# Performance work log

Hardware: AMD Instinct MI355X
Metric: run time of the kernel (lower is better)

Reference implementation:

```python
import jax, jax.numpy as jnp
import numpy as np

EPS = 1e-08


def _glorot(key, shape):
    fan_in, fan_out = shape[0], shape[1]
    lim = jnp.sqrt(6.0 / (fan_in + fan_out)).astype(jnp.float32)
    return jax.random.uniform(key, shape, jnp.float32, -lim, lim)


def setup_inputs() -> dict:
    key = jax.random.key(0)
    ks = jax.random.split(key, 12)
    n_nodes, n_edges, nf, hid = 50000, 1600000, 64, 64
    x = jax.random.normal(ks[0], (n_nodes, 3), jnp.float32)
    hh = jax.random.normal(ks[1], (n_nodes, nf), jnp.float32)
    src_idx = jax.random.randint(ks[2], (n_edges,), 0, n_nodes)
    dst_idx = jax.random.randint(ks[3], (n_edges,), 0, n_nodes)
    in_edge = 2 * nf + 1  # radial (1) + src hh + dst hh
    params = {
        "W1": _glorot(ks[4], (in_edge, hid)), "b1": jnp.zeros((hid,), jnp.float32),
        "W2": _glorot(ks[5], (hid, hid)),     "b2": jnp.zeros((hid,), jnp.float32),
        "W3": _glorot(ks[6], (hid, hid)),     "b3": jnp.zeros((hid,), jnp.float32),
        # final coord layer: xavier_uniform with gain 0.001, no bias
        "W4": _glorot(ks[7], (hid, 1)) * 0.001,
    }
    return {"x": x, "hh": hh, "src_idx": src_idx, "dst_idx": dst_idx, **params}


def reference(x, hh, src_idx, dst_idx, W1, b1, W2, b2, W3, b3, W4):
    # gather per-edge endpoint data
    xs, xd = x[src_idx], x[dst_idx]              # [E,3]
    coord_diff = xs - xd                         # [E,3]
    radial = jnp.sum(coord_diff * coord_diff, axis=1, keepdims=True)  # [E,1]

    # edge MLP: Linear -> SiLU -> Linear -> SiLU
    ef = jnp.concatenate([radial, hh[src_idx], hh[dst_idx]], axis=1)  # [E, 2*nf+1]
    ef = jax.nn.silu(ef @ W1 + b1)
    edge_feature = jax.nn.silu(ef @ W2 + b2)     # [E, hid]

    # normalize coord_diff by detached distance (normalize=True)
    norm = jax.lax.stop_gradient(jnp.sqrt(radial)) + EPS
    coord_diff = coord_diff / norm

    # coord MLP: Linear -> SiLU -> Linear(hid,1,no bias) -> Tanh (tanh=True)
    scale = jnp.tanh(jax.nn.silu(edge_feature @ W3 + b3) @ W4)  # [E,1]
    trans = coord_diff * scale                   # [E,3]
    return radial, trans, edge_feature
```

## Files before the change

kernel.cpp:

```cpp
#include <hip/hip_runtime.h>
#include <math.h>

typedef _Float16 f16x8 __attribute__((ext_vector_type(8)));
typedef __fp16   pk16x2 __attribute__((ext_vector_type(2)));
typedef float    f32x16 __attribute__((ext_vector_type(16)));
typedef float    f32x4  __attribute__((ext_vector_type(4)));
typedef unsigned int u32x4 __attribute__((ext_vector_type(4)));

__device__ __forceinline__ float silu_f(float v) {
  return v * __builtin_amdgcn_rcpf(1.0f + __expf(-v));
}
__device__ __forceinline__ float tanh_fast(float x) {
  return 1.0f - 2.0f * __builtin_amdgcn_rcpf(__expf(2.0f * x) + 1.0f);
}

__device__ __forceinline__ unsigned pkrtz(float a, float b) {
  pk16x2 h = __builtin_amdgcn_cvt_pkrtz(a, b);
  return __builtin_bit_cast(unsigned, h);
}
__device__ __forceinline__ void plswap(unsigned &a, unsigned &b) {
  asm volatile("v_permlane32_swap_b32 %0, %1" : "+v"(a), "+v"(b));
}
__device__ __forceinline__ f16x8 frag4(unsigned r0, unsigned r1, unsigned r2, unsigned r3) {
  u32x4 u = {r0, r1, r2, r3};
  return __builtin_bit_cast(f16x8, u);
}
__device__ __forceinline__ f32x16 zero16() {
  f32x16 z;
  #pragma unroll
  for (int i = 0; i < 16; ++i) z[i] = 0.0f;
  return z;
}

#define NFRAG 38

__global__ __launch_bounds__(512, 8) void egnn_edge_kernel(
    const float* __restrict__ x,
    const float* __restrict__ hh,
    const int* __restrict__ src_idx,
    const int* __restrict__ dst_idx,
    const float* __restrict__ W1, const float* __restrict__ b1,
    const float* __restrict__ W2, const float* __restrict__ b2,
    const float* __restrict__ W3, const float* __restrict__ b3,
    const float* __restrict__ W4,
    float* __restrict__ out_radial,
    float* __restrict__ out_trans,
    float* __restrict__ out_ef,
    int n_edges)
{
    __shared__ __align__(16) unsigned short sA[NFRAG * 512];
    __shared__ float sW4f[64];

    const int tid = threadIdx.x;

    for (int idx = tid; idx < NFRAG * 64; idx += 512) {
        const int f = idx >> 6, l = idx & 63;
        const int fhi = l >> 5, row = l & 31;
        int layer, m, t;
        if (f < 18)      { layer = 1; m = f / 9;        t = f % 9; }
        else if (f < 28) { layer = 2; m = (f - 18) / 5; t = (f - 18) % 5; }
        else             { layer = 3; m = (f - 28) / 5; t = (f - 28) % 5; }
        const int row_out = m * 32 + row;
        #pragma unroll
        for (int j = 0; j < 8; ++j) {
            const int kf = t * 16 + fhi * 8 + j;
            float v = 0.0f;
            if (layer == 1) {
                if (kf < 128)       v = W1[(1 + kf) * 64 + row_out];
                else if (kf == 128) v = W1[row_out];
                else if (kf == 136) v = b1[row_out];
            } else {
                const float* W = (layer == 2) ? W2 : W3;
                const float* b = (layer == 2) ? b2 : b3;
                if (kf < 64)       v = W[kf * 64 + row_out];
                else if (kf == 64) v = b[row_out];
            }
            sA[f * 512 + l * 8 + j] = __builtin_bit_cast(unsigned short, (_Float16)v);
        }
    }
    for (int i = tid; i < 64; i += 512) {
        const int fhi = i >> 5, k = i & 31;
        const int m = k >> 4, r = k & 15;
        sW4f[i] = W4[m * 32 + (r & 3) + 8 * (r >> 2) + 4 * fhi];
    }
    __syncthreads();

    const int lane = tid & 63;
    const int c  = lane & 31;
    const int hi = lane >> 5;
    const int wave = tid >> 6;
    const unsigned short* myA = sA + lane * 8;

    const long ngrp = ((long)n_edges + 31) >> 5;
    const long wid  = (long)blockIdx.x * 8 + wave;
    const long wtot = (long)gridDim.x * 8;

    for (long g = wid; g < ngrp; g += wtot) {
        const long eidx = g * 32 + c;
        const long e = (eidx < n_edges) ? eidx : (long)n_edges - 1;
        const bool valid = (eidx < n_edges);
        const int s = src_idx[e];
        const int d = dst_idx[e];

        const float dx0 = x[3*s+0] - x[3*d+0];
        const float dx1 = x[3*s+1] - x[3*d+1];
        const float dx2 = x[3*s+2] - x[3*d+2];
        const float radial = dx0*dx0 + dx1*dx1 + dx2*dx2;

        const float4* hsp = reinterpret_cast<const float4*>(hh + (long)s * 64 + hi * 8);
        const float4* hdp = reinterpret_cast<const float4*>(hh + (long)d * 64 + hi * 8);
        unsigned B1[9][4];
        #pragma unroll
        for (int t = 0; t < 4; ++t) {
            float4 a = hsp[4*t], b = hsp[4*t + 1];
            B1[t][0] = pkrtz(a.x, a.y); B1[t][1] = pkrtz(a.z, a.w);
            B1[t][2] = pkrtz(b.x, b.y); B1[t][3] = pkrtz(b.z, b.w);
            float4 p = hdp[4*t], q = hdp[4*t + 1];
            B1[4+t][0] = pkrtz(p.x, p.y); B1[4+t][1] = pkrtz(p.z, p.w);
            B1[4+t][2] = pkrtz(q.x, q.y); B1[4+t][3] = pkrtz(q.z, q.w);
        }
        B1[8][0] = hi ? 0x00003C00u : pkrtz(radial, 0.0f);
        B1[8][1] = 0u; B1[8][2] = 0u; B1[8][3] = 0u;

        f32x16 acc0 = zero16(), acc1 = zero16();
        #pragma unroll
        for (int t = 0; t < 9; ++t) {
            f16x8 bt = frag4(B1[t][0], B1[t][1], B1[t][2], B1[t][3]);
            acc0 = __builtin_amdgcn_mfma_f32_32x32x16_f16(
                *(const f16x8*)(myA + (t)     * 512), bt, acc0, 0, 0, 0);
            acc1 = __builtin_amdgcn_mfma_f32_32x32x16_f16(
                *(const f16x8*)(myA + (9 + t) * 512), bt, acc1, 0, 0, 0);
        }
        f32x16 s0, s1;
        #pragma unroll
        for (int r = 0; r < 16; ++r) { s0[r] = silu_f(acc0[r]); s1[r] = silu_f(acc1[r]); }

        unsigned B2[4][4];
        #pragma unroll
        for (int tt = 0; tt < 2; ++tt) {
            unsigned L0 = pkrtz(s0[8*tt+0], s0[8*tt+1]), L1 = pkrtz(s0[8*tt+2], s0[8*tt+3]);
            unsigned H0 = pkrtz(s0[8*tt+4], s0[8*tt+5]), H1 = pkrtz(s0[8*tt+6], s0[8*tt+7]);
            plswap(L0, H0); plswap(L1, H1);
            B2[tt][0] = L0; B2[tt][1] = L1; B2[tt][2] = H0; B2[tt][3] = H1;
            unsigned M0 = pkrtz(s1[8*tt+0], s1[8*tt+1]), M1 = pkrtz(s1[8*tt+2], s1[8*tt+3]);
            unsigned N0 = pkrtz(s1[8*tt+4], s1[8*tt+5]), N1 = pkrtz(s1[8*tt+6], s1[8*tt+7]);
            plswap(M0, N0); plswap(M1, N1);
            B2[2+tt][0] = M0; B2[2+tt][1] = M1; B2[2+tt][2] = N0; B2[2+tt][3] = N1;
        }

        const unsigned bias_b0 = hi ? 0u : 0x00003C00u;
        f32x16 a20 = zero16(), a21 = zero16();
        #pragma unroll
        for (int t = 0; t < 4; ++t) {
            f16x8 bt = frag4(B2[t][0], B2[t][1], B2[t][2], B2[t][3]);
            a20 = __builtin_amdgcn_mfma_f32_32x32x16_f16(
                *(const f16x8*)(myA + (18 + t) * 512), bt, a20, 0, 0, 0);
            a21 = __builtin_amdgcn_mfma_f32_32x32x16_f16(
                *(const f16x8*)(myA + (23 + t) * 512), bt, a21, 0, 0, 0);
        }
        {
            f16x8 bb = frag4(bias_b0, 0u, 0u, 0u);
            a20 = __builtin_amdgcn_mfma_f32_32x32x16_f16(
                *(const f16x8*)(myA + 22 * 512), bb, a20, 0, 0, 0);
            a21 = __builtin_amdgcn_mfma_f32_32x32x16_f16(
                *(const f16x8*)(myA + 27 * 512), bb, a21, 0, 0, 0);
        }
        f32x16 e0s, e1s;
        #pragma unroll
        for (int r = 0; r < 16; ++r) { e0s[r] = silu_f(a20[r]); e1s[r] = silu_f(a21[r]); }

        if (valid) {
            float* efp = out_ef + e * 64 + hi * 4;
            #pragma unroll
            for (int q = 0; q < 4; ++q) {
                f32x4 v0 = {e0s[4*q+0], e0s[4*q+1], e0s[4*q+2], e0s[4*q+3]};
                f32x4 v1 = {e1s[4*q+0], e1s[4*q+1], e1s[4*q+2], e1s[4*q+3]};
                __builtin_nontemporal_store(v0, reinterpret_cast<f32x4*>(efp + 8*q));
                __builtin_nontemporal_store(v1, reinterpret_cast<f32x4*>(efp + 32 + 8*q));
            }
        }

        unsigned B3[4][4];
        #pragma unroll
        for (int tt = 0; tt < 2; ++tt) {
            unsigned L0 = pkrtz(e0s[8*tt+0], e0s[8*tt+1]), L1 = pkrtz(e0s[8*tt+2], e0s[8*tt+3]);
            unsigned H0 = pkrtz(e0s[8*tt+4], e0s[8*tt+5]), H1 = pkrtz(e0s[8*tt+6], e0s[8*tt+7]);
            plswap(L0, H0); plswap(L1, H1);
            B3[tt][0] = L0; B3[tt][1] = L1; B3[tt][2] = H0; B3[tt][3] = H1;
            unsigned M0 = pkrtz(e1s[8*tt+0], e1s[8*tt+1]), M1 = pkrtz(e1s[8*tt+2], e1s[8*tt+3]);
            unsigned N0 = pkrtz(e1s[8*tt+4], e1s[8*tt+5]), N1 = pkrtz(e1s[8*tt+6], e1s[8*tt+7]);
            plswap(M0, N0); plswap(M1, N1);
            B3[2+tt][0] = M0; B3[2+tt][1] = M1; B3[2+tt][2] = N0; B3[2+tt][3] = N1;
        }
        f32x16 a30 = zero16(), a31 = zero16();
        #pragma unroll
        for (int t = 0; t < 4; ++t) {
            f16x8 bt = frag4(B3[t][0], B3[t][1], B3[t][2], B3[t][3]);
            a30 = __builtin_amdgcn_mfma_f32_32x32x16_f16(
                *(const f16x8*)(myA + (28 + t) * 512), bt, a30, 0, 0, 0);
            a31 = __builtin_amdgcn_mfma_f32_32x32x16_f16(
                *(const f16x8*)(myA + (33 + t) * 512), bt, a31, 0, 0, 0);
        }
        {
            f16x8 bb = frag4(bias_b0, 0u, 0u, 0u);
            a30 = __builtin_amdgcn_mfma_f32_32x32x16_f16(
                *(const f16x8*)(myA + 32 * 512), bb, a30, 0, 0, 0);
            a31 = __builtin_amdgcn_mfma_f32_32x32x16_f16(
                *(const f16x8*)(myA + 37 * 512), bb, a31, 0, 0, 0);
        }

        float partial = 0.0f;
        const float4* w4p = reinterpret_cast<const float4*>(sW4f + hi * 32);
        #pragma unroll
        for (int q = 0; q < 4; ++q) {
            const float4 w0 = w4p[q];
            const float4 w1 = w4p[4 + q];
            partial = fmaf(silu_f(a30[4*q+0]), w0.x, partial);
            partial = fmaf(silu_f(a30[4*q+1]), w0.y, partial);
            partial = fmaf(silu_f(a30[4*q+2]), w0.z, partial);
            partial = fmaf(silu_f(a30[4*q+3]), w0.w, partial);
            partial = fmaf(silu_f(a31[4*q+0]), w1.x, partial);
            partial = fmaf(silu_f(a31[4*q+1]), w1.y, partial);
            partial = fmaf(silu_f(a31[4*q+2]), w1.z, partial);
            partial = fmaf(silu_f(a31[4*q+3]), w1.w, partial);
        }
        const float tot = partial + __shfl_xor(partial, 32);
        const float scale = tanh_fast(tot);

        if (valid && hi == 0) {
            __builtin_nontemporal_store(radial, out_radial + e);
            const float k = scale * __builtin_amdgcn_rcpf(sqrtf(radial) + 1e-8f);
            __builtin_nontemporal_store(dx0 * k, out_trans + e*3 + 0);
            __builtin_nontemporal_store(dx1 * k, out_trans + e*3 + 1);
            __builtin_nontemporal_store(dx2 * k, out_trans + e*3 + 2);
        }
    }
}

extern "C" void kernel_launch(void* const* d_in, const int* in_sizes, int n_in,
                              void* d_out, int out_size, void* d_ws, size_t ws_size,
                              hipStream_t stream) {
    const float* x   = (const float*)d_in[0];
    const float* hh  = (const float*)d_in[1];
    const int* src_idx = (const int*)d_in[2];
    const int* dst_idx = (const int*)d_in[3];
    const float* W1  = (const float*)d_in[4];
    const float* b1  = (const float*)d_in[5];
    const float* W2  = (const float*)d_in[6];
    const float* b2  = (const float*)d_in[7];
    const float* W3  = (const float*)d_in[8];
    const float* b3  = (const float*)d_in[9];
    const float* W4  = (const float*)d_in[10];

    const int E = in_sizes[2];

    float* out_radial = (float*)d_out;
    float* out_trans  = out_radial + (long)E;
    float* out_ef     = out_radial + (long)E * 4;

    dim3 grid(2048), block(512);
    egnn_edge_kernel<<<grid, block, 0, stream>>>(
        x, hh, src_idx, dst_idx, W1, b1, W2, b2, W3, b3, W4,
        out_radial, out_trans, out_ef, E);
}
```

Before: 788.8 us.

## Software-pipeline gathers of next edge group across MLP stages

Prefetches the next group's indices and endpoint features and the index pair two groups ahead, issuing the hh gathers between MFMA stages so gather latency overlaps compute. Bias fragments for W1/b2/b3 move from shared memory into registers computed once per wave. Launch bounds drop from 8 to 4 blocks per CU and the grid is sized to give about six groups per wave. The extra live registers for the prefetched data lower occupancy, which may reduce the latency hiding that came from having more waves.

```diff
diff --git a/kernel.cpp b/kernel.cpp
--- a/kernel.cpp
+++ b/kernel.cpp
@@ -13,7 +13,6 @@
 __device__ __forceinline__ float tanh_fast(float x) {
   return 1.0f - 2.0f * __builtin_amdgcn_rcpf(__expf(2.0f * x) + 1.0f);
 }
-
 __device__ __forceinline__ unsigned pkrtz(float a, float b) {
   pk16x2 h = __builtin_amdgcn_cvt_pkrtz(a, b);
   return __builtin_bit_cast(unsigned, h);
@@ -31,10 +30,11 @@
   for (int i = 0; i < 16; ++i) z[i] = 0.0f;
   return z;
 }
+#define MFMA32 __builtin_amdgcn_mfma_f32_32x32x16_f16
 
 #define NFRAG 38
 
-__global__ __launch_bounds__(512, 8) void egnn_edge_kernel(
+__global__ __launch_bounds__(512, 4) void egnn_edge_kernel(
     const float* __restrict__ x,
     const float* __restrict__ hh,
     const int* __restrict__ src_idx,
@@ -94,42 +94,74 @@
     const long ngrp = ((long)n_edges + 31) >> 5;
     const long wid  = (long)blockIdx.x * 8 + wave;
     const long wtot = (long)gridDim.x * 8;
+    if (wid >= ngrp) return;
+
+    const unsigned frA8_m0 = pkrtz(hi ? b1[c]      : W1[c],      0.0f);
+    const unsigned frA8_m1 = pkrtz(hi ? b1[32 + c] : W1[32 + c], 0.0f);
+    const unsigned fb2m0 = hi ? 0u : pkrtz(b2[c],      0.0f);
+    const unsigned fb2m1 = hi ? 0u : pkrtz(b2[32 + c], 0.0f);
+    const unsigned fb3m0 = hi ? 0u : pkrtz(b3[c],      0.0f);
+    const unsigned fb3m1 = hi ? 0u : pkrtz(b3[32 + c], 0.0f);
+    const unsigned bias_b0 = hi ? 0u : 0x00003C00u;
+
+    unsigned Bc[8][4]; unsigned Bc8;
+    float dxc0, dxc1, dxc2, radc;
+    {
+        long e0 = wid * 32 + c; if (e0 >= n_edges) e0 = n_edges - 1;
+        const int s0 = src_idx[e0], d0 = dst_idx[e0];
+        dxc0 = x[3*s0+0] - x[3*d0+0];
+        dxc1 = x[3*s0+1] - x[3*d0+1];
+        dxc2 = x[3*s0+2] - x[3*d0+2];
+        radc = dxc0*dxc0 + dxc1*dxc1 + dxc2*dxc2;
+        const float4* hsp = reinterpret_cast<const float4*>(hh + (long)s0 * 64 + hi * 8);
+        const float4* hdp = reinterpret_cast<const float4*>(hh + (long)d0 * 64 + hi * 8);
+        #pragma unroll
+        for (int t = 0; t < 4; ++t) {
+            float4 a = hsp[4*t], b = hsp[4*t + 1];
+            Bc[t][0] = pkrtz(a.x, a.y); Bc[t][1] = pkrtz(a.z, a.w);
+            Bc[t][2] = pkrtz(b.x, b.y); Bc[t][3] = pkrtz(b.z, b.w);
+            float4 p = hdp[4*t], q = hdp[4*t + 1];
+            Bc[4+t][0] = pkrtz(p.x, p.y); Bc[4+t][1] = pkrtz(p.z, p.w);
+            Bc[4+t][2] = pkrtz(q.x, q.y); Bc[4+t][3] = pkrtz(q.z, q.w);
+        }
+        Bc8 = hi ? 0x00003C00u : pkrtz(radc, 0.0f);
+    }
+    int sn, dn;
+    {
+        long g1 = wid + wtot; if (g1 >= ngrp) g1 = wid;
+        long e1 = g1 * 32 + c; if (e1 >= n_edges) e1 = n_edges - 1;
+        sn = src_idx[e1]; dn = dst_idx[e1];
+    }
 
     for (long g = wid; g < ngrp; g += wtot) {
         const long eidx = g * 32 + c;
         const long e = (eidx < n_edges) ? eidx : (long)n_edges - 1;
         const bool valid = (eidx < n_edges);
-        const int s = src_idx[e];
-        const int d = dst_idx[e];
-
-        const float dx0 = x[3*s+0] - x[3*d+0];
-        const float dx1 = x[3*s+1] - x[3*d+1];
-        const float dx2 = x[3*s+2] - x[3*d+2];
-        const float radial = dx0*dx0 + dx1*dx1 + dx2*dx2;
-
-        const float4* hsp = reinterpret_cast<const float4*>(hh + (long)s * 64 + hi * 8);
-        const float4* hdp = reinterpret_cast<const float4*>(hh + (long)d * 64 + hi * 8);
-        unsigned B1[9][4];
-        #pragma unroll
-        for (int t = 0; t < 4; ++t) {
-            float4 a = hsp[4*t], b = hsp[4*t + 1];
-            B1[t][0] = pkrtz(a.x, a.y); B1[t][1] = pkrtz(a.z, a.w);
-            B1[t][2] = pkrtz(b.x, b.y); B1[t][3] = pkrtz(b.z, b.w);
-            float4 p = hdp[4*t], q = hdp[4*t + 1];
-            B1[4+t][0] = pkrtz(p.x, p.y); B1[4+t][1] = pkrtz(p.z, p.w);
-            B1[4+t][2] = pkrtz(q.x, q.y); B1[4+t][3] = pkrtz(q.z, q.w);
-        }
-        B1[8][0] = hi ? 0x00003C00u : pkrtz(radial, 0.0f);
-        B1[8][1] = 0u; B1[8][2] = 0u; B1[8][3] = 0u;
+
+        const float* hsb = hh + (long)sn * 64 + hi * 8;
+        f32x4 nhs[8];
+        #pragma unroll
+        for (int t = 0; t < 4; ++t) {
+            nhs[2*t]   = *reinterpret_cast<const f32x4*>(hsb + 16*t);
+            nhs[2*t+1] = *reinterpret_cast<const f32x4*>(hsb + 16*t + 4);
+        }
+        const float nxs0 = x[3*sn+0], nxs1 = x[3*sn+1], nxs2 = x[3*sn+2];
+        const float nxd0 = x[3*dn+0], nxd1 = x[3*dn+1], nxd2 = x[3*dn+2];
+        long g2 = g + 2*wtot; if (g2 >= ngrp) g2 = ngrp - 1;
+        long e2 = g2 * 32 + c; if (e2 >= n_edges) e2 = n_edges - 1;
+        const int s2 = src_idx[e2], d2 = dst_idx[e2];
 
         f32x16 acc0 = zero16(), acc1 = zero16();
         #pragma unroll
-        for (int t = 0; t < 9; ++t) {
-            f16x8 bt = frag4(B1[t][0], B1[t][1], B1[t][2], B1[t][3]);
-            acc0 = __builtin_amdgcn_mfma_f32_32x32x16_f16(
-                *(const f16x8*)(myA + (t)     * 512), bt, acc0, 0, 0, 0);
-            acc1 = __builtin_amdgcn_mfma_f32_32x32x16_f16(
-                *(const f16x8*)(myA + (9 + t) * 512), bt, acc1, 0, 0, 0);
+        for (int t = 0; t < 8; ++t) {
+            f16x8 bt = frag4(Bc[t][0], Bc[t][1], Bc[t][2], Bc[t][3]);
+            acc0 = MFMA32(*(const f16x8*)(myA + (t)     * 512), bt, acc0, 0, 0, 0);
+            acc1 = MFMA32(*(const f16x8*)(myA + (9 + t) * 512), bt, acc1, 0, 0, 0);
+        }
+        {
+            f16x8 bt = frag4(Bc8, 0u, 0u, 0u);
+            acc0 = MFMA32(frag4(frA8_m0, 0u, 0u, 0u), bt, acc0, 0, 0, 0);
+            acc1 = MFMA32(frag4(frA8_m1, 0u, 0u, 0u), bt, acc1, 0, 0, 0);
         }
         f32x16 s0, s1;
         #pragma unroll
@@ -148,22 +180,17 @@
             B2[2+tt][0] = M0; B2[2+tt][1] = M1; B2[2+tt][2] = N0; B2[2+tt][3] = N1;
         }
 
-        const unsigned bias_b0 = hi ? 0u : 0x00003C00u;
         f32x16 a20 = zero16(), a21 = zero16();
         #pragma unroll
         for (int t = 0; t < 4; ++t) {
             f16x8 bt = frag4(B2[t][0], B2[t][1], B2[t][2], B2[t][3]);
-            a20 = __builtin_amdgcn_mfma_f32_32x32x16_f16(
-                *(const f16x8*)(myA + (18 + t) * 512), bt, a20, 0, 0, 0);
-            a21 = __builtin_amdgcn_mfma_f32_32x32x16_f16(
-                *(const f16x8*)(myA + (23 + t) * 512), bt, a21, 0, 0, 0);
+            a20 = MFMA32(*(const f16x8*)(myA + (18 + t) * 512), bt, a20, 0, 0, 0);
+            a21 = MFMA32(*(const f16x8*)(myA + (23 + t) * 512), bt, a21, 0, 0, 0);
         }
         {
             f16x8 bb = frag4(bias_b0, 0u, 0u, 0u);
-            a20 = __builtin_amdgcn_mfma_f32_32x32x16_f16(
-                *(const f16x8*)(myA + 22 * 512), bb, a20, 0, 0, 0);
-            a21 = __builtin_amdgcn_mfma_f32_32x32x16_f16(
-                *(const f16x8*)(myA + 27 * 512), bb, a21, 0, 0, 0);
+            a20 = MFMA32(frag4(fb2m0, 0u, 0u, 0u), bb, a20, 0, 0, 0);
+            a21 = MFMA32(frag4(fb2m1, 0u, 0u, 0u), bb, a21, 0, 0, 0);
         }
         f32x16 e0s, e1s;
         #pragma unroll
@@ -180,6 +207,25 @@
             }
         }
 
+        unsigned Bn0[4][4]; unsigned Bn8;
+        #pragma unroll
+        for (int t = 0; t < 4; ++t) {
+            Bn0[t][0] = pkrtz(nhs[2*t].x,   nhs[2*t].y);
+            Bn0[t][1] = pkrtz(nhs[2*t].z,   nhs[2*t].w);
+            Bn0[t][2] = pkrtz(nhs[2*t+1].x, nhs[2*t+1].y);
+            Bn0[t][3] = pkrtz(nhs[2*t+1].z, nhs[2*t+1].w);
+        }
+        const float dxn0 = nxs0 - nxd0, dxn1 = nxs1 - nxd1, dxn2 = nxs2 - nxd2;
+        const float radn = dxn0*dxn0 + dxn1*dxn1 + dxn2*dxn2;
+        Bn8 = hi ? 0x00003C00u : pkrtz(radn, 0.0f);
+        const float* hdb = hh + (long)dn * 64 + hi * 8;
+        f32x4 nhd[8];
+        #pragma unroll
+        for (int t = 0; t < 4; ++t) {
+            nhd[2*t]   = *reinterpret_cast<const f32x4*>(hdb + 16*t);
+            nhd[2*t+1] = *reinterpret_cast<const f32x4*>(hdb + 16*t + 4);
+        }
+
         unsigned B3[4][4];
         #pragma unroll
         for (int tt = 0; tt < 2; ++tt) {
@@ -196,17 +242,13 @@
         #pragma unroll
         for (int t = 0; t < 4; ++t) {
             f16x8 bt = frag4(B3[t][0], B3[t][1], B3[t][2], B3[t][3]);
-            a30 = __builtin_amdgcn_mfma_f32_32x32x16_f16(
-                *(const f16x8*)(myA + (28 + t) * 512), bt, a30, 0, 0, 0);
-            a31 = __builtin_amdgcn_mfma_f32_32x32x16_f16(
-                *(const f16x8*)(myA + (33 + t) * 512), bt, a31, 0, 0, 0);
+            a30 = MFMA32(*(const f16x8*)(myA + (28 + t) * 512), bt, a30, 0, 0, 0);
+            a31 = MFMA32(*(const f16x8*)(myA + (33 + t) * 512), bt, a31, 0, 0, 0);
         }
         {
             f16x8 bb = frag4(bias_b0, 0u, 0u, 0u);
-            a30 = __builtin_amdgcn_mfma_f32_32x32x16_f16(
-                *(const f16x8*)(myA + 32 * 512), bb, a30, 0, 0, 0);
-            a31 = __builtin_amdgcn_mfma_f32_32x32x16_f16(
-                *(const f16x8*)(myA + 37 * 512), bb, a31, 0, 0, 0);
+            a30 = MFMA32(frag4(fb3m0, 0u, 0u, 0u), bb, a30, 0, 0, 0);
+            a31 = MFMA32(frag4(fb3m1, 0u, 0u, 0u), bb, a31, 0, 0, 0);
         }
 
         float partial = 0.0f;
@@ -228,12 +270,25 @@
         const float scale = tanh_fast(tot);
 
         if (valid && hi == 0) {
-            __builtin_nontemporal_store(radial, out_radial + e);
-            const float k = scale * __builtin_amdgcn_rcpf(sqrtf(radial) + 1e-8f);
-            __builtin_nontemporal_store(dx0 * k, out_trans + e*3 + 0);
-            __builtin_nontemporal_store(dx1 * k, out_trans + e*3 + 1);
-            __builtin_nontemporal_store(dx2 * k, out_trans + e*3 + 2);
-        }
+            __builtin_nontemporal_store(radc, out_radial + e);
+            const float k = scale * __builtin_amdgcn_rcpf(sqrtf(radc) + 1e-8f);
+            __builtin_nontemporal_store(dxc0 * k, out_trans + e*3 + 0);
+            __builtin_nontemporal_store(dxc1 * k, out_trans + e*3 + 1);
+            __builtin_nontemporal_store(dxc2 * k, out_trans + e*3 + 2);
+        }
+
+        #pragma unroll
+        for (int t = 0; t < 4; ++t) {
+            Bc[t][0] = Bn0[t][0]; Bc[t][1] = Bn0[t][1];
+            Bc[t][2] = Bn0[t][2]; Bc[t][3] = Bn0[t][3];
+            Bc[4+t][0] = pkrtz(nhd[2*t].x,   nhd[2*t].y);
+            Bc[4+t][1] = pkrtz(nhd[2*t].z,   nhd[2*t].w);
+            Bc[4+t][2] = pkrtz(nhd[2*t+1].x, nhd[2*t+1].y);
+            Bc[4+t][3] = pkrtz(nhd[2*t+1].z, nhd[2*t+1].w);
+        }
+        Bc8 = Bn8;
+        dxc0 = dxn0; dxc1 = dxn1; dxc2 = dxn2; radc = radn;
+        sn = s2; dn = d2;
     }
 }
 
@@ -258,7 +313,11 @@
     float* out_trans  = out_radial + (long)E;
     float* out_ef     = out_radial + (long)E * 4;
 
-    dim3 grid(2048), block(512);
+    const long ngrp = ((long)E + 31) >> 5;
+    long blocks = (ngrp + 47) / 48;
+    if (blocks < 1) blocks = 1;
+    if (blocks > 8192) blocks = 8192;
+    dim3 grid((unsigned)blocks), block(512);
     egnn_edge_kernel<<<grid, block, 0, stream>>>(
         x, hh, src_idx, dst_idx, W1, b1, W2, b2, W3, b3, W4,
         out_radial, out_trans, out_ef, E);
```

Result: slower. 864.2 us (+9.6%).
